# Optimization experiments

Measured on AMD Instinct MI355X. Metric: run time of the kernel, lower is better.

The kernel has to match this reference:

```python
import jax, jax.numpy as jnp
import numpy as np

BLOCK = 64
EPS = 1e-6
N_HEADS = 16


def _rope(t, cos, sin):
    # t: (B,S,H,hd); cos/sin: (S, hd//2) -> broadcast (1,S,1,hd//2)
    B, S, H, hd = t.shape
    tr = t.reshape(B, S, H, hd // 2, 2)
    t0, t1 = tr[..., 0], tr[..., 1]
    c = cos[None, :, None, :]
    s = sin[None, :, None, :]
    o0 = t0 * c - t1 * s
    o1 = t0 * s + t1 * c
    return jnp.stack([o0, o1], axis=-1).reshape(B, S, H, hd)


def setup_inputs() -> dict:
    key = jax.random.key(0)
    ks = jax.random.split(key, 6)
    B, S, D = 1, 2048, 2048
    hd = D // N_HEADS
    x = jax.random.normal(ks[0], (B, S, D), dtype=jnp.float32)
    # rotary table: theta_i = 10000^(-2i/hd)
    inv_freq = 1.0 / (10000.0 ** (jnp.arange(0, hd, 2, dtype=jnp.float32) / hd))
    t = jnp.arange(S, dtype=jnp.float32)
    freqs = jnp.outer(t, inv_freq)  # (S, hd//2)
    freqs_cos = jnp.cos(freqs)
    freqs_sin = jnp.sin(freqs)
    std = 0.02
    Wq = jax.random.normal(ks[1], (D, D), dtype=jnp.float32) * std
    Wk = jax.random.normal(ks[2], (D, D), dtype=jnp.float32) * std
    Wv = jax.random.normal(ks[3], (D, D), dtype=jnp.float32) * std
    Wo = jax.random.normal(ks[4], (D, D), dtype=jnp.float32) * std
    mask = jnp.ones((1, 1), dtype=bool)  # non-None mask => no masking in original code
    return {"x": x, "freqs_cos": freqs_cos, "freqs_sin": freqs_sin,
            "Wq": Wq, "Wk": Wk, "Wv": Wv, "Wo": Wo, "mask": mask}


def reference(x, freqs_cos, freqs_sin, Wq, Wk, Wv, Wo, mask):
    B, S, D = x.shape
    H = N_HEADS
    hd = D // H
    scale = hd ** -0.5
    nb = S // BLOCK

    q = (x @ Wq.T).reshape(B, S, H, hd)
    k = (x @ Wk.T).reshape(B, S, H, hd)
    v = (x @ Wv.T).reshape(B, S, H, hd)
    q = _rope(q, freqs_cos, freqs_sin)
    k = _rope(k, freqs_cos, freqs_sin)

    # block views: (B, nb, BLOCK, H, hd)
    qb = q.reshape(B, nb, BLOCK, H, hd)
    kb = k.reshape(B, nb, BLOCK, H, hd)
    vb = v.reshape(B, nb, BLOCK, H, hd)

    # per-(i,j) block scores: (B, nb_i, nb_j, H, BLOCK_q, BLOCK_k)
    s = jnp.einsum('binhd,bjmhd->bijhnm', qb, kb) * scale
    # NOTE: original module (mask is not None path) applies NO causal mask and
    # uses the per-block local max (no running-max rescale) -- reproduced exactly.
    m = jnp.max(s, axis=-1, keepdims=True)
    p = jnp.exp(s - m)
    # denominator: sum of per-block row sums over all j blocks -> (B, nb, H, BLOCK)
    L = p.sum(axis=-1).sum(axis=2)
    # numerator: sum over j blocks of p @ v -> (B, nb, BLOCK, H, hd)
    O = jnp.einsum('bijhnm,bjmhd->binhd', p, vb).reshape(B, S, H, hd)
    Lr = L.transpose(0, 1, 3, 2).reshape(B, S, H, 1)  # (B,S,H,1)
    O = O / (Lr + EPS)
    return O.reshape(B, S, D) @ Wo.T
```

## Files before the change

kernel.cpp:

```cpp
#include <hip/hip_runtime.h>
#include <hip/hip_bf16.h>
#include <math.h>

#define SEQ 2048
#define DM  2048
#define NH  16
#define HD  128
#define SCALE 0.08838834764831845f

typedef __bf16 bf16_t;
typedef __bf16 bf16x8 __attribute__((ext_vector_type(8)));
typedef __bf16 bf16x4 __attribute__((ext_vector_type(4)));
typedef float  f32x4  __attribute__((ext_vector_type(4)));
typedef int    i32x4  __attribute__((ext_vector_type(4)));

typedef const __attribute__((address_space(1))) void* gas_ptr;
typedef __attribute__((address_space(3))) void* las_ptr;

__device__ __forceinline__ void gload_lds16(const void* g, void* l) {
    __builtin_amdgcn_global_load_lds((gas_ptr)g, (las_ptr)l, 16, 0, 0);
}

__device__ __forceinline__ f32x4 mfma_bf16(bf16x8 a, bf16x8 b, f32x4 c) {
    return __builtin_amdgcn_mfma_f32_16x16x32_bf16(a, b, c, 0, 0, 0);
}

__device__ __forceinline__ unsigned cvtpk_bf16(float lo, float hi) {
    unsigned d;
    asm("v_cvt_pk_bf16_f32 %0, %1, %2" : "=v"(d) : "v"(lo), "v"(hi));
    return d;
}

__device__ __forceinline__ bf16x8 read_frag64(const bf16_t* lds, int row, int k) {
    int chunk = (k >> 3) ^ (row & 7);
    return *(const bf16x8*)(lds + row * 64 + chunk * 8);
}
__device__ __forceinline__ bf16x8 read_frag128(const bf16_t* lds, int row, int k) {
    int chunk = k >> 3;
    chunk = (chunk & 8) | ((chunk ^ row) & 7);
    return *(const bf16x8*)(lds + row * 128 + chunk * 8);
}
__device__ __forceinline__ bf16x8 read_slab(const bf16_t* sl, int row, int g) {
    int j = g ^ ((row >> 1) & 3);
    return *(const bf16x8*)(sl + row * 32 + j * 8);
}

__global__ __launch_bounds__(256) void cvt5(
    const float* __restrict__ s0, const float* __restrict__ s1,
    const float* __restrict__ s2, const float* __restrict__ s3,
    const float* __restrict__ s4,
    bf16_t* __restrict__ d0, bf16_t* __restrict__ d1, bf16_t* __restrict__ d2,
    bf16_t* __restrict__ d3, bf16_t* __restrict__ d4)
{
    int which = blockIdx.y;
    const float* s; bf16_t* d;
    switch (which) {
        case 0: s = s0; d = d0; break;
        case 1: s = s1; d = d1; break;
        case 2: s = s2; d = d2; break;
        case 3: s = s3; d = d3; break;
        default: s = s4; d = d4; break;
    }
    size_t idx = ((size_t)blockIdx.x * 256 + threadIdx.x) * 4;
    float4 v = *(const float4*)(s + idx);
    bf16x4 o = { (bf16_t)v.x, (bf16_t)v.y, (bf16_t)v.z, (bf16_t)v.w };
    *(bf16x4*)(d + idx) = o;
}

__global__ __launch_bounds__(256, 3) void qkv_m97(
    const bf16_t* __restrict__ A, const bf16_t* __restrict__ Ball,
    bf16_t* __restrict__ Oq, bf16_t* __restrict__ Ok, bf16_t* __restrict__ Ov,
    const float* __restrict__ fcos, const float* __restrict__ fsin)
{
    __shared__ bf16_t lA[128 * 32];
    __shared__ bf16_t lB[128 * 32];

    const int tid = threadIdx.x;
    const int lane = tid & 63;
    const int w = tid >> 6;
    const int wm = w >> 1, wn = w & 1;
    const int g4 = lane >> 4, r15 = lane & 15;

    const int bn = blockIdx.x;
    const int bm = blockIdx.y;
    const int sel = bn >> 4;

    const size_t arow0 = (size_t)bm * 128;
    const size_t brow0 = (size_t)bn * 128;

    const int rw0 = tid >> 2,        kj0 = (tid & 3) ^ ((rw0 >> 1) & 3);
    const int rw1 = (256 + tid) >> 2, kj1 = ((256 + tid) & 3) ^ ((rw1 >> 1) & 3);
    const bf16_t* pA0 = A    + (arow0 + rw0) * DM + kj0 * 8;
    const bf16_t* pA1 = A    + (arow0 + rw1) * DM + kj1 * 8;
    const bf16_t* pB0 = Ball + (brow0 + rw0) * DM + kj0 * 8;
    const bf16_t* pB1 = Ball + (brow0 + rw1) * DM + kj1 * 8;
    char* dA0 = (char*)lA + tid * 16;
    char* dA1 = (char*)lA + (256 + tid) * 16;
    char* dB0 = (char*)lB + tid * 16;
    char* dB1 = (char*)lB + (256 + tid) * 16;

    f32x4 acc[4][4] = {};

    for (int kt = 0; kt < DM / 32; ++kt) {
        const int k0 = kt * 32;
        gload_lds16(pA0 + k0, dA0);
        gload_lds16(pA1 + k0, dA1);
        gload_lds16(pB0 + k0, dB0);
        gload_lds16(pB1 + k0, dB1);
        __syncthreads();

        bf16x8 af[4], bfr[4];
        #pragma unroll
        for (int m = 0; m < 4; ++m)
            af[m] = read_slab(lA, wm * 64 + m * 16 + r15, g4);
        #pragma unroll
        for (int n = 0; n < 4; ++n)
            bfr[n] = read_slab(lB, wn * 64 + n * 16 + r15, g4);
        #pragma unroll
        for (int m = 0; m < 4; ++m)
            #pragma unroll
            for (int n = 0; n < 4; ++n)
                acc[m][n] = mfma_bf16(af[m], bfr[n], acc[m][n]);
        __syncthreads();
    }

    const int r0 = bm * 128 + wm * 64;
    const int c0g = bn * 128 + wn * 64;

    if (sel == 2) {
        #pragma unroll
        for (int m = 0; m < 4; ++m) {
            int rowb = r0 + m * 16 + g4 * 4;
            #pragma unroll
            for (int n = 0; n < 4; ++n) {
                int colr = (c0g + n * 16 + r15) & 2047;
                bf16x4 pk = { (bf16_t)acc[m][n][0], (bf16_t)acc[m][n][1],
                              (bf16_t)acc[m][n][2], (bf16_t)acc[m][n][3] };
                *(bf16x4*)&Ov[(size_t)colr * SEQ + rowb] = pk;
            }
        }
    } else {
        bf16_t* dst = (sel == 0) ? Oq : Ok;
        #pragma unroll
        for (int m = 0; m < 4; ++m) {
            int rowb = r0 + m * 16 + g4 * 4;
            #pragma unroll
            for (int n = 0; n < 4; ++n) {
                int colr = (c0g + n * 16 + r15) & 2047;
                int f = (colr & (HD - 1)) >> 1;
                float sgn = (colr & 1) ? 1.0f : -1.0f;
                #pragma unroll
                for (int r = 0; r < 4; ++r) {
                    float mine = acc[m][n][r];
                    float other = __shfl_xor(mine, 1);
                    float cc = fcos[(rowb + r) * (HD / 2) + f];
                    float ss = fsin[(rowb + r) * (HD / 2) + f];
                    float o = mine * cc + sgn * other * ss;
                    dst[(size_t)(rowb + r) * DM + colr] = (bf16_t)o;
                }
            }
        }
    }
}

__global__ __launch_bounds__(256) void gemm_fin(
    const bf16_t* __restrict__ A, const bf16_t* __restrict__ B0,
    float* __restrict__ Of)
{
    __shared__ bf16_t lA[128 * 64];
    __shared__ bf16_t lB[64 * 64];

    const int tid = threadIdx.x;
    const int lane = tid & 63;
    const int w = tid >> 6;
    const int wm = w >> 1, wn = w & 1;
    const int g = lane >> 4, r15 = lane & 15;

    const int bm = blockIdx.x;
    const int bn = blockIdx.y;

    f32x4 acc[4][2] = {};

    const size_t arow0 = (size_t)bm * 128;
    const size_t brow0 = (size_t)bn * 64;

    for (int kt = 0; kt < DM / 64; ++kt) {
        const int k0 = kt * 64;
        #pragma unroll
        for (int i = 0; i < 4; ++i) {
            int c = i * 256 + tid;
            int row = c >> 3;
            int ck = (c ^ row) & 7;
            const bf16_t* ga = A + (arow0 + row) * DM + k0 + ck * 8;
            gload_lds16(ga, (char*)lA + (i * 256 + w * 64) * 16);
        }
        #pragma unroll
        for (int i = 0; i < 2; ++i) {
            int c = i * 256 + tid;
            int row = c >> 3;
            int ck = (c ^ row) & 7;
            const bf16_t* gb = B0 + (brow0 + row) * DM + k0 + ck * 8;
            gload_lds16(gb, (char*)lB + (i * 256 + w * 64) * 16);
        }
        __syncthreads();
        #pragma unroll
        for (int kk = 0; kk < 2; ++kk) {
            bf16x8 af[4], bfr[2];
            #pragma unroll
            for (int m = 0; m < 4; ++m)
                af[m] = read_frag64(lA, wm * 64 + m * 16 + r15, kk * 32 + g * 8);
            #pragma unroll
            for (int n = 0; n < 2; ++n)
                bfr[n] = read_frag64(lB, wn * 32 + n * 16 + r15, kk * 32 + g * 8);
            #pragma unroll
            for (int m = 0; m < 4; ++m)
                #pragma unroll
                for (int n = 0; n < 2; ++n)
                    acc[m][n] = mfma_bf16(af[m], bfr[n], acc[m][n]);
        }
        __syncthreads();
    }

    const int r0 = bm * 128 + wm * 64;
    const int c0 = bn * 64 + wn * 32;
    #pragma unroll
    for (int m = 0; m < 4; ++m) {
        int rowb = r0 + m * 16 + g * 4;
        #pragma unroll
        for (int n = 0; n < 2; ++n) {
            int col = c0 + n * 16 + r15;
            #pragma unroll
            for (int r = 0; r < 4; ++r)
                Of[(size_t)(rowb + r) * DM + col] = acc[m][n][r];
        }
    }
}

__global__ __launch_bounds__(256, 2) void attn_k6(
    const bf16_t* __restrict__ Q, const bf16_t* __restrict__ Kb,
    const bf16_t* __restrict__ Vt, bf16_t* __restrict__ Op,
    float* __restrict__ Lp)
{
    __shared__ bf16_t lk[2 * 64 * 128];
    __shared__ bf16_t lv[2 * 128 * 64];

    const int tid = threadIdx.x;
    const int lane = tid & 63;
    const int w = tid >> 6;
    const int g = lane >> 4, r15 = lane & 15;
    const int qb = blockIdx.x;
    const int h = blockIdx.y;
    const int sp = blockIdx.z;
    const int j0 = sp * 16;

    const int lo = g & 1, hb = g >> 1;
    const int e_src = (lo << 5) + r15;
    const int o_src = e_src + 16;
    const int sA = hb ? o_src : e_src;
    const int sB = hb ? e_src : o_src;

    bf16x8 qf[2][4];
    #pragma unroll
    for (int u = 0; u < 2; ++u) {
        const bf16_t* qrow = Q + (size_t)(qb * 128 + w * 32 + u * 16 + r15) * DM + h * HD + g * 8;
        #pragma unroll
        for (int ks = 0; ks < 4; ++ks)
            qf[u][ks] = *(const bf16x8*)(qrow + ks * 32);
    }

    f32x4 oacc[2][8] = {};
    float Lsum[2] = {0.f, 0.f};

    #define STAGE_KV(JJ, BUF)                                                     \
    {                                                                             \
        _Pragma("unroll")                                                         \
        for (int i = 0; i < 4; ++i) {                                             \
            int c = i * 256 + tid;                                                \
            int row = c >> 4, ckl = c & 15;                                       \
            int ck = (ckl & 8) | ((ckl ^ row) & 7);                               \
            const bf16_t* gk = Kb + (size_t)((JJ) * 64 + row) * DM + h * HD + ck * 8; \
            gload_lds16(gk, (char*)lk + (BUF) * 16384 + (i * 256 + w * 64) * 16); \
        }                                                                         \
        _Pragma("unroll")                                                         \
        for (int i = 0; i < 4; ++i) {                                             \
            int c = i * 256 + tid;                                                \
            int row = c >> 3;                                                     \
            int ck = (c ^ row) & 7;                                               \
            const bf16_t* gv = Vt + (size_t)(h * HD + row) * SEQ + (JJ) * 64 + ck * 8; \
            gload_lds16(gv, (char*)lv + (BUF) * 16384 + (i * 256 + w * 64) * 16); \
        }                                                                         \
    }

    STAGE_KV(j0, 0);
    asm volatile("s_waitcnt vmcnt(0)" ::: "memory");
    __builtin_amdgcn_s_barrier();

    for (int jj = 0; jj < 16; ++jj) {
        const int cur = jj & 1;
        const bf16_t* lkc = lk + cur * 8192;
        const bf16_t* lvc = lv + cur * 8192;
        if (jj < 15) STAGE_KV(j0 + jj + 1, cur ^ 1);

        f32x4 sacc[2][4] = {};
        __builtin_amdgcn_s_setprio(1);
        #pragma unroll
        for (int ks = 0; ks < 4; ++ks) {
            #pragma unroll
            for (int n = 0; n < 4; ++n) {
                bf16x8 kf = read_frag128(lkc, n * 16 + r15, ks * 32 + g * 8);
                sacc[0][n] = mfma_bf16(kf, qf[0][ks], sacc[0][n]);
                sacc[1][n] = mfma_bf16(kf, qf[1][ks], sacc[1][n]);
            }
        }
        __builtin_amdgcn_s_setprio(0);

        bf16x8 pa0[2], pa1[2];
        #pragma unroll
        for (int u = 0; u < 2; ++u) {
            float mx0 = fmaxf(fmaxf(sacc[u][0][0], sacc[u][0][1]), fmaxf(sacc[u][0][2], sacc[u][0][3]));
            float mx1 = fmaxf(fmaxf(sacc[u][1][0], sacc[u][1][1]), fmaxf(sacc[u][1][2], sacc[u][1][3]));
            float mx2 = fmaxf(fmaxf(sacc[u][2][0], sacc[u][2][1]), fmaxf(sacc[u][2][2], sacc[u][2][3]));
            float mx3 = fmaxf(fmaxf(sacc[u][3][0], sacc[u][3][1]), fmaxf(sacc[u][3][2], sacc[u][3][3]));
            float mx = fmaxf(fmaxf(mx0, mx1), fmaxf(mx2, mx3));
            mx = fmaxf(mx, __shfl_xor(mx, 16));
            mx = fmaxf(mx, __shfl_xor(mx, 32));

            float p[4][4];
            float ls = 0.f;
            #pragma unroll
            for (int n = 0; n < 4; ++n)
                #pragma unroll
                for (int r = 0; r < 4; ++r) {
                    float pv = __expf((sacc[u][n][r] - mx) * SCALE);
                    p[n][r] = pv;
                    ls += pv;
                }
            Lsum[u] += ls;

            unsigned D00 = cvtpk_bf16(p[0][0], p[0][1]), D01 = cvtpk_bf16(p[0][2], p[0][3]);
            unsigned D10 = cvtpk_bf16(p[1][0], p[1][1]), D11 = cvtpk_bf16(p[1][2], p[1][3]);
            unsigned D20 = cvtpk_bf16(p[2][0], p[2][1]), D21 = cvtpk_bf16(p[2][2], p[2][3]);
            unsigned D30 = cvtpk_bf16(p[3][0], p[3][1]), D31 = cvtpk_bf16(p[3][2], p[3][3]);

            unsigned r0 = __shfl((int)(lo ? D10 : D00), sA);
            unsigned r1 = __shfl((int)(lo ? D11 : D01), sA);
            unsigned r2 = __shfl((int)(lo ? D00 : D10), sB);
            unsigned r3 = __shfl((int)(lo ? D01 : D11), sB);
            unsigned r4 = __shfl((int)(lo ? D30 : D20), sA);
            unsigned r5 = __shfl((int)(lo ? D31 : D21), sA);
            unsigned r6 = __shfl((int)(lo ? D20 : D30), sB);
            unsigned r7 = __shfl((int)(lo ? D21 : D31), sB);
            i32x4 w0, w1;
            w0[0] = (int)(hb ? r2 : r0);  w0[1] = (int)(hb ? r3 : r1);
            w0[2] = (int)(hb ? r0 : r2);  w0[3] = (int)(hb ? r1 : r3);
            w1[0] = (int)(hb ? r6 : r4);  w1[1] = (int)(hb ? r7 : r5);
            w1[2] = (int)(hb ? r4 : r6);  w1[3] = (int)(hb ? r5 : r7);
            pa0[u] = __builtin_bit_cast(bf16x8, w0);
            pa1[u] = __builtin_bit_cast(bf16x8, w1);
        }

        __builtin_amdgcn_s_setprio(1);
        #pragma unroll
        for (int n = 0; n < 8; ++n) {
            bf16x8 bv0 = read_frag64(lvc, n * 16 + r15, g * 8);
            oacc[0][n] = mfma_bf16(pa0[0], bv0, oacc[0][n]);
            oacc[1][n] = mfma_bf16(pa0[1], bv0, oacc[1][n]);
            bf16x8 bv1 = read_frag64(lvc, n * 16 + r15, 32 + g * 8);
            oacc[0][n] = mfma_bf16(pa1[0], bv1, oacc[0][n]);
            oacc[1][n] = mfma_bf16(pa1[1], bv1, oacc[1][n]);
        }
        __builtin_amdgcn_s_setprio(0);

        asm volatile("s_waitcnt vmcnt(0)" ::: "memory");
        __builtin_amdgcn_s_barrier();
    }

    #pragma unroll
    for (int u = 0; u < 2; ++u) {
        float L = Lsum[u];
        L += __shfl_xor(L, 16);
        L += __shfl_xor(L, 32);
        int qrow = qb * 128 + w * 32 + u * 16;
        if (g == 0)
            Lp[((size_t)sp * NH + h) * SEQ + qrow + r15] = L;

        #pragma unroll
        for (int n = 0; n < 8; ++n) {
            int col = h * HD + n * 16 + r15;
            int rowb = qrow + g * 4;
            #pragma unroll
            for (int r = 0; r < 4; ++r)
                Op[(size_t)sp * SEQ * DM + (size_t)(rowb + r) * DM + col] = (bf16_t)oacc[u][n][r];
        }
    }
}

__global__ __launch_bounds__(256) void attn_cmb(
    const bf16_t* __restrict__ Op, const float* __restrict__ Lp,
    bf16_t* __restrict__ Ob)
{
    const int row = blockIdx.x;
    const int c0 = threadIdx.x * 8;
    const int h = c0 >> 7;

    float L = 1e-6f;
    #pragma unroll
    for (int s = 0; s < 2; ++s)
        L += Lp[((size_t)s * NH + h) * SEQ + row];

    float acc[8] = {};
    #pragma unroll
    for (int s = 0; s < 2; ++s) {
        bf16x8 v = *(const bf16x8*)(Op + (size_t)s * SEQ * DM + (size_t)row * DM + c0);
        #pragma unroll
        for (int j = 0; j < 8; ++j)
            acc[j] += (float)v[j];
    }
    float inv = 1.0f / L;
    bf16x8 o;
    #pragma unroll
    for (int j = 0; j < 8; ++j)
        o[j] = (bf16_t)(acc[j] * inv);
    *(bf16x8*)(Ob + (size_t)row * DM + c0) = o;
}

extern "C" void kernel_launch(void* const* d_in, const int* in_sizes, int n_in,
                              void* d_out, int out_size, void* d_ws, size_t ws_size,
                              hipStream_t stream)
{
    const float* x    = (const float*)d_in[0];
    const float* fcos = (const float*)d_in[1];
    const float* fsin = (const float*)d_in[2];
    const float* Wq   = (const float*)d_in[3];
    const float* Wk   = (const float*)d_in[4];
    const float* Wv   = (const float*)d_in[5];
    const float* Wo   = (const float*)d_in[6];
    float* out = (float*)d_out;

    const size_t NE = (size_t)DM * SEQ;
    bf16_t* ws  = (bf16_t*)d_ws;
    bf16_t* xb  = ws;
    bf16_t* wqb = ws + 1 * NE;
    bf16_t* wkb = ws + 2 * NE;
    bf16_t* wvb = ws + 3 * NE;
    bf16_t* wob = ws + 4 * NE;
    bf16_t* qr  = ws + 5 * NE;
    bf16_t* kr  = ws + 6 * NE;
    bf16_t* vt  = ws + 7 * NE;
    bf16_t* ob  = ws + 8 * NE;
    bf16_t* op  = ws;
    float*  lp  = (float*)(ws + 9 * NE);

    hipLaunchKernelGGL(cvt5, dim3(4096, 5), dim3(256), 0, stream,
                       x, Wq, Wk, Wv, Wo, xb, wqb, wkb, wvb, wob);

    hipLaunchKernelGGL(qkv_m97, dim3(48, 16), dim3(256), 0, stream,
                       xb, wqb, qr, kr, vt, fcos, fsin);

    hipLaunchKernelGGL(attn_k6, dim3(16, 16, 2), dim3(256), 0, stream,
                       qr, kr, vt, op, lp);

    hipLaunchKernelGGL(attn_cmb, dim3(2048), dim3(256), 0, stream,
                       op, lp, ob);

    hipLaunchKernelGGL(gemm_fin, dim3(16, 32), dim3(256), 0, stream,
                       ob, wob, out);
}
```

Baseline: 170.0 us.

## Double-buffer LDS tiles in QKV GEMM to overlap global loads with MFMA

The QKV projection GEMM now uses two LDS buffers per operand and issues the global-to-LDS loads for the next k-tile before computing on the current one, with one waitcnt+barrier per iteration instead of two syncthreads. It also raises wave priority around the MFMA block. This is meant to hide global load latency behind matrix math, at the cost of doubled LDS usage (32KB per block), which may reduce occupancy under the launch bound of 3.

```diff
diff --git a/kernel.cpp b/kernel.cpp
--- a/kernel.cpp
+++ b/kernel.cpp
@@ -72,8 +72,8 @@
     bf16_t* __restrict__ Oq, bf16_t* __restrict__ Ok, bf16_t* __restrict__ Ov,
     const float* __restrict__ fcos, const float* __restrict__ fsin)
 {
-    __shared__ bf16_t lA[128 * 32];
-    __shared__ bf16_t lB[128 * 32];
+    __shared__ bf16_t lAb[2 * 4096];
+    __shared__ bf16_t lBb[2 * 4096];
 
     const int tid = threadIdx.x;
     const int lane = tid & 63;
@@ -88,41 +88,55 @@
     const size_t arow0 = (size_t)bm * 128;
     const size_t brow0 = (size_t)bn * 128;
 
-    const int rw0 = tid >> 2,        kj0 = (tid & 3) ^ ((rw0 >> 1) & 3);
+    const int rw0 = tid >> 2,         kj0 = (tid & 3) ^ ((rw0 >> 1) & 3);
     const int rw1 = (256 + tid) >> 2, kj1 = ((256 + tid) & 3) ^ ((rw1 >> 1) & 3);
     const bf16_t* pA0 = A    + (arow0 + rw0) * DM + kj0 * 8;
     const bf16_t* pA1 = A    + (arow0 + rw1) * DM + kj1 * 8;
     const bf16_t* pB0 = Ball + (brow0 + rw0) * DM + kj0 * 8;
     const bf16_t* pB1 = Ball + (brow0 + rw1) * DM + kj1 * 8;
-    char* dA0 = (char*)lA + tid * 16;
-    char* dA1 = (char*)lA + (256 + tid) * 16;
-    char* dB0 = (char*)lB + tid * 16;
-    char* dB1 = (char*)lB + (256 + tid) * 16;
+
+    #define STAGE_QKV(KT, BUF)                                          \
+    {                                                                   \
+        char* bA = (char*)lAb + (BUF) * 8192 + tid * 16;                \
+        char* bB = (char*)lBb + (BUF) * 8192 + tid * 16;                \
+        const int ko = (KT) * 32;                                       \
+        gload_lds16(pA0 + ko, bA);                                      \
+        gload_lds16(pA1 + ko, bA + 4096);                               \
+        gload_lds16(pB0 + ko, bB);                                      \
+        gload_lds16(pB1 + ko, bB + 4096);                               \
+    }
 
     f32x4 acc[4][4] = {};
 
+    STAGE_QKV(0, 0);
+    asm volatile("s_waitcnt vmcnt(0)" ::: "memory");
+    __builtin_amdgcn_s_barrier();
+
     for (int kt = 0; kt < DM / 32; ++kt) {
-        const int k0 = kt * 32;
-        gload_lds16(pA0 + k0, dA0);
-        gload_lds16(pA1 + k0, dA1);
-        gload_lds16(pB0 + k0, dB0);
-        gload_lds16(pB1 + k0, dB1);
-        __syncthreads();
-
+        const int cur = kt & 1;
+        if (kt < DM / 32 - 1) STAGE_QKV(kt + 1, cur ^ 1);
+
+        const bf16_t* sA = lAb + cur * 4096;
+        const bf16_t* sB = lBb + cur * 4096;
         bf16x8 af[4], bfr[4];
         #pragma unroll
         for (int m = 0; m < 4; ++m)
-            af[m] = read_slab(lA, wm * 64 + m * 16 + r15, g4);
+            af[m] = read_slab(sA, wm * 64 + m * 16 + r15, g4);
         #pragma unroll
         for (int n = 0; n < 4; ++n)
-            bfr[n] = read_slab(lB, wn * 64 + n * 16 + r15, g4);
+            bfr[n] = read_slab(sB, wn * 64 + n * 16 + r15, g4);
+        __builtin_amdgcn_s_setprio(1);
         #pragma unroll
         for (int m = 0; m < 4; ++m)
             #pragma unroll
             for (int n = 0; n < 4; ++n)
                 acc[m][n] = mfma_bf16(af[m], bfr[n], acc[m][n]);
-        __syncthreads();
-    }
+        __builtin_amdgcn_s_setprio(0);
+
+        asm volatile("s_waitcnt vmcnt(0)" ::: "memory");
+        __builtin_amdgcn_s_barrier();
+    }
+    #undef STAGE_QKV
 
     const int r0 = bm * 128 + wm * 64;
     const int c0g = bn * 128 + wn * 64;
```

After: 170.1 us. No clear change (+0.0%).
